# Kernel tuning notes

Hardware: AMD Instinct MI355X
Metric: run time of the kernel (lower is better)

## Reference

```python
import jax, jax.numpy as jnp
import numpy as np
import math

B, S, D, H = 4, 1024, 1024, 16
DK = D // H
WINDOW = 128
NEG = -100000.0


def setup_inputs() -> dict:
    key = jax.random.key(0)
    kx, kw1, kb1, kw2, kb2 = jax.random.split(key, 5)
    x = jax.random.normal(kx, (B, S, D), dtype=jnp.float32)
    # sliding-window band mask: True where |i-j| <= WINDOW
    i = jnp.arange(S)
    band = (jnp.abs(i[:, None] - i[None, :]) <= WINDOW)
    mask = jnp.broadcast_to(band, (B, S, S))
    # second structured mask: causal
    causal = (i[:, None] >= i[None, :])
    mask2 = jnp.broadcast_to(causal, (B, S, S))
    scale = 1.0 / math.sqrt(D)
    Wqkv = jax.random.normal(kw1, (D, 3 * D), dtype=jnp.float32) * scale
    bqkv = jax.random.normal(kb1, (3 * D,), dtype=jnp.float32) * 0.01
    Wo = jax.random.normal(kw2, (D, D), dtype=jnp.float32) * scale
    bo = jax.random.normal(kb2, (D,), dtype=jnp.float32) * 0.01
    return {"x": x, "mask": mask, "mask2": mask2, "Wqkv": Wqkv, "bqkv": bqkv, "Wo": Wo, "bo": bo}


def reference(x, mask, mask2, Wqkv, bqkv, Wo, bo):
    b, s, d = x.shape
    qkv = x @ Wqkv + bqkv                      # [b, s, 3d]
    q, k, v = jnp.split(qkv, 3, axis=-1)
    # [b, s, h, dk] -> [b, h, s, dk]
    q = q.reshape(b, s, H, DK).transpose(0, 2, 1, 3)
    k = k.reshape(b, s, H, DK).transpose(0, 2, 1, 3)
    v = v.reshape(b, s, H, DK).transpose(0, 2, 1, 3)
    scores = jnp.einsum('bhtd,bhsd->bhts', q, k) / math.sqrt(DK)
    scores = jnp.where(mask[:, None, :, :], scores, NEG)
    scores = jnp.where(mask2[:, None, :, :], scores, NEG)
    weights = jax.nn.softmax(scores, axis=-1)  # [b, h, t, s]
    context = jnp.einsum('bhts,bhsd->bhtd', weights, v)
    context = context.transpose(0, 2, 1, 3).reshape(b, s, d)
    context = context @ Wo + bo
    return (context, weights)
```

## Files before the change

### kernel.cpp

```cpp
#include <hip/hip_runtime.h>

typedef short bf16x8 __attribute__((ext_vector_type(8)));
typedef float floatx4 __attribute__((ext_vector_type(4)));

#define GLOBAL_AS __attribute__((address_space(1)))
#define LDS_AS __attribute__((address_space(3)))

__device__ __forceinline__ void gload_lds16(const ushort* g, ushort* l) {
  __builtin_amdgcn_global_load_lds((const GLOBAL_AS void*)g, (LDS_AS void*)l, 16, 0, 0);
}

__device__ __forceinline__ ushort f2bf(float x) {
  uint u = __float_as_uint(x);
  return (ushort)((u + 0x7fffu + ((u >> 16) & 1u)) >> 16);
}

__global__ __launch_bounds__(256) void k_prep(const float4* __restrict__ x, ushort4* __restrict__ xbf,
                                              const float* __restrict__ W1, ushort* __restrict__ O1,
                                              const float* __restrict__ W2, ushort* __restrict__ O2) {
  int bx = blockIdx.x;
  if (bx < 4096) {
    int g = bx * 256 + threadIdx.x;
    float4 v = x[g];
    ushort4 o;
    o.x = f2bf(v.x); o.y = f2bf(v.y); o.z = f2bf(v.z); o.w = f2bf(v.w);
    xbf[g] = o;
    return;
  }
  __shared__ float tile[32][33];
  int tb = bx - 4096;
  int by = tb >> 7, bxx = tb & 127;
  const float* in; ushort* out; int N;
  if (bxx < 96) { in = W1; out = O1; N = 3072; }
  else          { in = W2; out = O2; N = 1024; bxx -= 96; }
  const int K = 1024;
  int n0 = bxx * 32, k0 = by * 32;
  int tx = threadIdx.x & 31, ty = threadIdx.x >> 5;
  #pragma unroll
  for (int r = ty; r < 32; r += 8)
    tile[r][tx] = in[(size_t)(k0 + r) * N + n0 + tx];
  __syncthreads();
  #pragma unroll
  for (int r = ty; r < 32; r += 8)
    out[(size_t)(n0 + r) * K + k0 + tx] = f2bf(tile[tx][r]);
}

template <int OUT_BF16, int BN>
__global__ __launch_bounds__(256) void k_gemm_bt(const ushort* __restrict__ A,
                                                 const ushort* __restrict__ Bt,
                                                 const float* __restrict__ bias,
                                                 void* __restrict__ Cout,
                                                 int M, int N, int K) {
  constexpr int NI = BN / 32;
  constexpr int NB = BN / 64;
  __shared__ ushort As[128 * 32];
  __shared__ ushort Bs[BN * 32];
  const int t = threadIdx.x;
  const int m0 = blockIdx.y * 128, n0 = blockIdx.x * BN;
  const int w = t >> 6, l = t & 63;
  const int wm = (w & 1) * 64, wn = (w >> 1) * (BN / 2);
  const int lr = l & 15, q8 = (l >> 4) * 8;
  const int lrow = l >> 2, lcol = (l & 3) * 8;

  floatx4 acc[4][NI];
  #pragma unroll
  for (int i = 0; i < 4; ++i)
    #pragma unroll
    for (int j = 0; j < NI; ++j) acc[i][j] = (floatx4){0.f, 0.f, 0.f, 0.f};

  for (int k0 = 0; k0 < K; k0 += 32) {
    __syncthreads();
    #pragma unroll
    for (int i = 0; i < 2; ++i) {
      int r0 = (w * 2 + i) * 16;
      gload_lds16(A + (size_t)(m0 + r0 + lrow) * K + k0 + lcol, As + r0 * 32);
    }
    #pragma unroll
    for (int i = 0; i < NB; ++i) {
      int r0 = (w * NB + i) * 16;
      gload_lds16(Bt + (size_t)(n0 + r0 + lrow) * K + k0 + lcol, Bs + r0 * 32);
    }
    __syncthreads();
    bf16x8 af[4], bfr[NI];
    #pragma unroll
    for (int mi = 0; mi < 4; ++mi)
      af[mi] = *(const bf16x8*)(As + (wm + mi * 16 + lr) * 32 + q8);
    #pragma unroll
    for (int ni = 0; ni < NI; ++ni)
      bfr[ni] = *(const bf16x8*)(Bs + (wn + ni * 16 + lr) * 32 + q8);
    #pragma unroll
    for (int mi = 0; mi < 4; ++mi)
      #pragma unroll
      for (int ni = 0; ni < NI; ++ni)
        acc[mi][ni] = __builtin_amdgcn_mfma_f32_16x16x32_bf16(af[mi], bfr[ni], acc[mi][ni], 0, 0, 0);
  }

  const int rq = (l >> 4) * 4;
  #pragma unroll
  for (int ni = 0; ni < NI; ++ni) {
    int col = n0 + wn + ni * 16 + lr;
    float bv = bias[col];
    #pragma unroll
    for (int mi = 0; mi < 4; ++mi) {
      int row = m0 + wm + mi * 16 + rq;
      #pragma unroll
      for (int r2 = 0; r2 < 4; ++r2) {
        float v = acc[mi][ni][r2] + bv;
        size_t idx = (size_t)(row + r2) * N + col;
        if (OUT_BF16) ((ushort*)Cout)[idx] = f2bf(v);
        else          ((float*)Cout)[idx] = v;
      }
    }
  }
}

__global__ __launch_bounds__(256) void k_attn(const ushort* __restrict__ qkv,
                                              float* __restrict__ wout,
                                              ushort* __restrict__ ctxout) {
  __shared__ ushort smKP[192 * 68];
  __shared__ ushort smVT[64 * 200];
  __shared__ float smInv[64];

  const int t = threadIdx.x;
  const int w = t >> 6, l = t & 63;
  const int lr = l & 15, q8 = (l >> 4) * 8, q4 = (l >> 4) * 4;
  const int iblk = blockIdx.x & 15;
  const int h = (blockIdx.x >> 4) & 15;
  const int b = blockIdx.x >> 8;
  const int i0 = iblk * 64;
  const int jb0 = i0 - 128;
  const int tok0 = b * 1024 + i0;
  const int qoff = h * 64, koff = 1024 + h * 64, voff = 2048 + h * 64;
  const size_t wbase = ((size_t)(b * 16 + h) * 1024 + i0) * 1024;

  {
    int scol = ((l & 7) ^ (l >> 3)) * 8;
    #pragma unroll
    for (int c = 0; c < 6; ++c) {
      int r0 = (c * 4 + w) * 8;
      int jsrc = jb0 + r0 + (l >> 3); if (jsrc < 0) jsrc = 0;
      gload_lds16(qkv + (size_t)(b * 1024 + jsrc) * 3072 + koff + scol, smKP + r0 * 64);
    }
  }
  #pragma unroll
  for (int c = 0; c < 6; ++c) {
    int idx = t + 256 * c;
    int j = (idx & 15) + 16 * (idx >> 7);
    int d0 = ((idx >> 4) & 7) * 8;
    int jsrc = jb0 + j; if (jsrc < 0) jsrc = 0;
    uint4 u = *(const uint4*)(qkv + (size_t)(b * 1024 + jsrc) * 3072 + voff + d0);
    ushort* p = smVT + j;
    p[(d0 + 0) * 200] = (ushort)(u.x & 0xffffu);
    p[(d0 + 1) * 200] = (ushort)(u.x >> 16);
    p[(d0 + 2) * 200] = (ushort)(u.y & 0xffffu);
    p[(d0 + 3) * 200] = (ushort)(u.y >> 16);
    p[(d0 + 4) * 200] = (ushort)(u.z & 0xffffu);
    p[(d0 + 5) * 200] = (ushort)(u.z >> 16);
    p[(d0 + 6) * 200] = (ushort)(u.w & 0xffffu);
    p[(d0 + 7) * 200] = (ushort)(u.w >> 16);
  }

  const ushort* qrow = qkv + (size_t)(tok0 + w * 16 + lr) * 3072 + qoff;
  bf16x8 aq0 = *(const bf16x8*)(qrow + q8);
  bf16x8 aq1 = *(const bf16x8*)(qrow + 32 + q8);
  __syncthreads();

  const int kc0 = q8 ^ ((lr & 7) << 3);
  const int kc1 = (q8 + 32) ^ ((lr & 7) << 3);
  floatx4 sc[12];
  #pragma unroll
  for (int ni = 0; ni < 12; ++ni) sc[ni] = (floatx4){0.f, 0.f, 0.f, 0.f};
  #pragma unroll
  for (int ni = 0; ni < 12; ++ni) {
    bf16x8 bk0 = *(const bf16x8*)(smKP + (ni * 16 + lr) * 64 + kc0);
    bf16x8 bk1 = *(const bf16x8*)(smKP + (ni * 16 + lr) * 64 + kc1);
    sc[ni] = __builtin_amdgcn_mfma_f32_16x16x32_bf16(aq0, bk0, sc[ni], 0, 0, 0);
    sc[ni] = __builtin_amdgcn_mfma_f32_16x16x32_bf16(aq1, bk1, sc[ni], 0, 0, 0);
  }
  __syncthreads();

  float mrow[4] = {-3e38f, -3e38f, -3e38f, -3e38f};
  #pragma unroll
  for (int ni = 0; ni < 12; ++ni) {
    int nj = ni * 16 + lr;
    #pragma unroll
    for (int reg = 0; reg < 4; ++reg) {
      int di = w * 16 + q4 + reg;
      bool valid = (nj >= di) & (nj <= di + 128) & (jb0 + nj >= 0);
      float s = valid ? sc[ni][reg] * 0.125f : -3e38f;
      sc[ni][reg] = s;
      mrow[reg] = fmaxf(mrow[reg], s);
    }
  }
  #pragma unroll
  for (int reg = 0; reg < 4; ++reg) {
    #pragma unroll
    for (int off = 1; off < 16; off <<= 1)
      mrow[reg] = fmaxf(mrow[reg], __shfl_xor(mrow[reg], off, 64));
  }
  float lrow[4] = {0.f, 0.f, 0.f, 0.f};
  #pragma unroll
  for (int ni = 0; ni < 12; ++ni) {
    #pragma unroll
    for (int reg = 0; reg < 4; ++reg) {
      float e = __expf(sc[ni][reg] - mrow[reg]);
      sc[ni][reg] = e;
      lrow[reg] += e;
    }
  }
  float inv[4];
  #pragma unroll
  for (int reg = 0; reg < 4; ++reg) {
    float s = lrow[reg];
    #pragma unroll
    for (int off = 1; off < 16; off <<= 1) s += __shfl_xor(s, off, 64);
    inv[reg] = 1.0f / s;
  }

  ushort* smP = smKP;
  #pragma unroll
  for (int ni = 0; ni < 12; ++ni) {
    int nj = ni * 16 + lr;
    #pragma unroll
    for (int reg = 0; reg < 4; ++reg) {
      int il = w * 16 + q4 + reg;
      smP[il * 204 + nj] = f2bf(sc[ni][reg]);
    }
  }
  if (lr == 0) {
    #pragma unroll
    for (int reg = 0; reg < 4; ++reg) smInv[w * 16 + q4 + reg] = inv[reg];
  }
  __syncthreads();

  {
    const int j4 = t * 4;
    const unsigned nj4 = (unsigned)(j4 - jb0);
    const bool inband = nj4 < 192u;
    const int njc = inband ? (int)nj4 : 0;
    const float bandf = inband ? 1.0f : 0.0f;
    float* wp = wout + wbase + j4;
    const ushort* pp = smP + njc;
    #pragma unroll 4
    for (int r = 0; r < 64; ++r) {
      ushort4 pv = *(const ushort4*)(pp + r * 204);
      float iv = smInv[r] * bandf;
      floatx4 o = { __uint_as_float((uint)pv.x << 16) * iv,
                    __uint_as_float((uint)pv.y << 16) * iv,
                    __uint_as_float((uint)pv.z << 16) * iv,
                    __uint_as_float((uint)pv.w << 16) * iv };
      __builtin_nontemporal_store(o, (floatx4*)(wp + (size_t)r * 1024));
    }
  }

  floatx4 oc[4];
  #pragma unroll
  for (int ni = 0; ni < 4; ++ni) oc[ni] = (floatx4){0.f, 0.f, 0.f, 0.f};
  #pragma unroll
  for (int ks = 0; ks < 6; ++ks) {
    bf16x8 ap = *(const bf16x8*)(smP + (w * 16 + lr) * 204 + ks * 32 + q8);
    #pragma unroll
    for (int ni = 0; ni < 4; ++ni) {
      bf16x8 bv = *(const bf16x8*)(smVT + (ni * 16 + lr) * 200 + ks * 32 + q8);
      oc[ni] = __builtin_amdgcn_mfma_f32_16x16x32_bf16(ap, bv, oc[ni], 0, 0, 0);
    }
  }

  #pragma unroll
  for (int ni = 0; ni < 4; ++ni) {
    int d = ni * 16 + lr;
    #pragma unroll
    for (int reg = 0; reg < 4; ++reg) {
      int il = w * 16 + q4 + reg;
      ctxout[(size_t)(tok0 + il) * 1024 + qoff + d] = f2bf(oc[ni][reg] * inv[reg]);
    }
  }
}

extern "C" void kernel_launch(void* const* d_in, const int* in_sizes, int n_in,
                              void* d_out, int out_size, void* d_ws, size_t ws_size,
                              hipStream_t stream) {
  const float* x    = (const float*)d_in[0];
  const float* Wqkv = (const float*)d_in[3];
  const float* bqkv = (const float*)d_in[4];
  const float* Wo   = (const float*)d_in[5];
  const float* bo   = (const float*)d_in[6];

  float* out_ctx = (float*)d_out;
  float* out_w   = out_ctx + (size_t)4 * 1024 * 1024;

  char* ws = (char*)d_ws;
  ushort* qkv_bf = (ushort*)(ws);
  ushort* ctx_bf = (ushort*)(ws + 25165824);
  ushort* x_bf   = (ushort*)(ws + 33554432);
  ushort* WqkvT  = (ushort*)(ws + 41943040);
  ushort* WoT    = (ushort*)(ws + 48234496);

  k_prep<<<8192, 256, 0, stream>>>((const float4*)x, (ushort4*)x_bf, Wqkv, WqkvT, Wo, WoT);
  k_gemm_bt<1, 128><<<dim3(24, 32), 256, 0, stream>>>(x_bf, WqkvT, bqkv, qkv_bf, 4096, 3072, 1024);
  k_attn<<<1024, 256, 0, stream>>>(qkv_bf, out_w, ctx_bf);
  k_gemm_bt<0, 64><<<dim3(16, 32), 256, 0, stream>>>(ctx_bf, WoT, bo, out_ctx, 4096, 1024, 1024);
}
```

Baseline: 397.1 us.

## Overlap zero-fill of attention weights with QKV GEMM blocks

Moves the zero-writing of the out-of-band part of the weights matrix out of the attention kernel and into extra blocks interleaved with the QKV GEMM. The aim is to overlap the bandwidth-bound zero stores with the compute-bound GEMM. The attention kernel now writes only the in-band columns of each row. The cost is a custom block-index mapping, extra grid blocks, and a duplicated GEMM body.

New measurement: 1.039 ms. 162% more time.

```diff
diff --git a/kernel.cpp b/kernel.cpp
--- a/kernel.cpp
+++ b/kernel.cpp
@@ -45,11 +45,97 @@
     out[(size_t)(n0 + r) * K + k0 + tx] = f2bf(tile[tx][r]);
 }
 
-template <int OUT_BF16, int BN>
+__global__ __launch_bounds__(256) void k_gemm1_z(const ushort* __restrict__ A,
+                                                 const ushort* __restrict__ Bt,
+                                                 const float* __restrict__ bias,
+                                                 ushort* __restrict__ Cout,
+                                                 float* __restrict__ wout) {
+  __shared__ ushort As[128 * 32];
+  __shared__ ushort Bs[128 * 32];
+  const int t = threadIdx.x;
+  const int bid = blockIdx.x;
+  const int rr = bid % 7, cc = bid / 7;
+
+  if (rr >= 3) {
+    int z = cc * 4 + (rr - 3);
+    int i0 = (z & 15) * 64;
+    int sstart = i0 - 128 < 0 ? 0 : i0 - 128;
+    int send = i0 + 64;
+    int s4 = sstart >> 2, e4 = send >> 2;
+    int nper = (1024 - (send - sstart)) >> 4;
+    size_t wb = ((size_t)((z >> 8) * 16 + ((z >> 4) & 15)) * 1024 + i0) * 1024;
+    float* wp = wout + wb + (size_t)(t >> 2) * 1024;
+    int q = t & 3;
+    floatx4 zf = {0.f, 0.f, 0.f, 0.f};
+    for (int i = 0; i < nper; ++i) {
+      int zf4 = q * nper + i;
+      int c4 = zf4 < s4 ? zf4 : zf4 + (e4 - s4);
+      __builtin_nontemporal_store(zf, (floatx4*)(wp + c4 * 4));
+    }
+    return;
+  }
+
+  const int g = cc * 3 + rr;
+  const int m0 = (g / 24) * 128, n0 = (g % 24) * 128;
+  const int N = 3072, K = 1024;
+  const int w = t >> 6, l = t & 63;
+  const int wm = (w & 1) * 64, wn = (w >> 1) * 64;
+  const int lr = l & 15, q8 = (l >> 4) * 8;
+  const int lrow = l >> 2, lcol = (l & 3) * 8;
+
+  floatx4 acc[4][4];
+  #pragma unroll
+  for (int i = 0; i < 4; ++i)
+    #pragma unroll
+    for (int j = 0; j < 4; ++j) acc[i][j] = (floatx4){0.f, 0.f, 0.f, 0.f};
+
+  for (int k0 = 0; k0 < K; k0 += 32) {
+    __syncthreads();
+    #pragma unroll
+    for (int i = 0; i < 2; ++i) {
+      int r0 = (w * 2 + i) * 16;
+      gload_lds16(A + (size_t)(m0 + r0 + lrow) * K + k0 + lcol, As + r0 * 32);
+    }
+    #pragma unroll
+    for (int i = 0; i < 2; ++i) {
+      int r0 = (w * 2 + i) * 16;
+      gload_lds16(Bt + (size_t)(n0 + r0 + lrow) * K + k0 + lcol, Bs + r0 * 32);
+    }
+    __syncthreads();
+    bf16x8 af[4], bfr[4];
+    #pragma unroll
+    for (int mi = 0; mi < 4; ++mi)
+      af[mi] = *(const bf16x8*)(As + (wm + mi * 16 + lr) * 32 + q8);
+    #pragma unroll
+    for (int ni = 0; ni < 4; ++ni)
+      bfr[ni] = *(const bf16x8*)(Bs + (wn + ni * 16 + lr) * 32 + q8);
+    #pragma unroll
+    for (int mi = 0; mi < 4; ++mi)
+      #pragma unroll
+      for (int ni = 0; ni < 4; ++ni)
+        acc[mi][ni] = __builtin_amdgcn_mfma_f32_16x16x32_bf16(af[mi], bfr[ni], acc[mi][ni], 0, 0, 0);
+  }
+
+  const int rq = (l >> 4) * 4;
+  #pragma unroll
+  for (int ni = 0; ni < 4; ++ni) {
+    int col = n0 + wn + ni * 16 + lr;
+    float bv = bias[col];
+    #pragma unroll
+    for (int mi = 0; mi < 4; ++mi) {
+      int row = m0 + wm + mi * 16 + rq;
+      #pragma unroll
+      for (int r2 = 0; r2 < 4; ++r2)
+        Cout[(size_t)(row + r2) * N + col] = f2bf(acc[mi][ni][r2] + bv);
+    }
+  }
+}
+
+template <int BN>
 __global__ __launch_bounds__(256) void k_gemm_bt(const ushort* __restrict__ A,
                                                  const ushort* __restrict__ Bt,
                                                  const float* __restrict__ bias,
-                                                 void* __restrict__ Cout,
+                                                 float* __restrict__ Cout,
                                                  int M, int N, int K) {
   constexpr int NI = BN / 32;
   constexpr int NB = BN / 64;
@@ -104,12 +190,8 @@
     for (int mi = 0; mi < 4; ++mi) {
       int row = m0 + wm + mi * 16 + rq;
       #pragma unroll
-      for (int r2 = 0; r2 < 4; ++r2) {
-        float v = acc[mi][ni][r2] + bv;
-        size_t idx = (size_t)(row + r2) * N + col;
-        if (OUT_BF16) ((ushort*)Cout)[idx] = f2bf(v);
-        else          ((float*)Cout)[idx] = v;
-      }
+      for (int r2 = 0; r2 < 4; ++r2)
+        Cout[(size_t)(row + r2) * N + col] = acc[mi][ni][r2] + bv;
     }
   }
 }
@@ -234,22 +316,23 @@
   __syncthreads();
 
   {
-    const int j4 = t * 4;
-    const unsigned nj4 = (unsigned)(j4 - jb0);
-    const bool inband = nj4 < 192u;
-    const int njc = inband ? (int)nj4 : 0;
-    const float bandf = inband ? 1.0f : 0.0f;
-    float* wp = wout + wbase + j4;
-    const ushort* pp = smP + njc;
-    #pragma unroll 4
-    for (int r = 0; r < 64; ++r) {
-      ushort4 pv = *(const ushort4*)(pp + r * 204);
-      float iv = smInv[r] * bandf;
+    const int sstart = jb0 < 0 ? 0 : jb0;
+    const int send = i0 + 64;
+    const int wq = (send - sstart) >> 4;
+    const int rrow = t >> 2, q = t & 3;
+    const float iv = smInv[rrow];
+    const ushort* pp = smP + rrow * 204;
+    float* wp = wout + wbase + (size_t)rrow * 1024;
+    const int c40 = (sstart >> 2) + q * wq;
+    for (int i = 0; i < wq; ++i) {
+      int c4 = c40 + i;
+      int nj = c4 * 4 - jb0;
+      ushort4 pv = *(const ushort4*)(pp + nj);
       floatx4 o = { __uint_as_float((uint)pv.x << 16) * iv,
                     __uint_as_float((uint)pv.y << 16) * iv,
                     __uint_as_float((uint)pv.z << 16) * iv,
                     __uint_as_float((uint)pv.w << 16) * iv };
-      __builtin_nontemporal_store(o, (floatx4*)(wp + (size_t)r * 1024));
+      __builtin_nontemporal_store(o, (floatx4*)(wp + c4 * 4));
     }
   }
 
@@ -297,7 +380,7 @@
   ushort* WoT    = (ushort*)(ws + 48234496);
 
   k_prep<<<8192, 256, 0, stream>>>((const float4*)x, (ushort4*)x_bf, Wqkv, WqkvT, Wo, WoT);
-  k_gemm_bt<1, 128><<<dim3(24, 32), 256, 0, stream>>>(x_bf, WqkvT, bqkv, qkv_bf, 4096, 3072, 1024);
+  k_gemm1_z<<<1792, 256, 0, stream>>>(x_bf, WqkvT, bqkv, qkv_bf, out_w);
   k_attn<<<1024, 256, 0, stream>>>(qkv_bf, out_w, ctx_bf);
-  k_gemm_bt<0, 64><<<dim3(16, 32), 256, 0, stream>>>(ctx_bf, WoT, bo, out_ctx, 4096, 1024, 1024);
-}
+  k_gemm_bt<64><<<dim3(16, 32), 256, 0, stream>>>(ctx_bf, WoT, bo, out_ctx, 4096, 1024, 1024);
+}
```
